# Kernel tuning notes

Measured on AMD Instinct MI355X. Metric: run time of the kernel, lower is better.

## Reference

```python
import jax, jax.numpy as jnp
import numpy as np

K = 5        # kernel_size
S = 1        # stride_size
EPS = 1e-5   # LayerNorm eps (torch default)


def setup_inputs() -> dict:
    key = jax.random.key(0)
    ks = jax.random.split(key, 5)
    N, C, H, W = 8, 512, 32, 32
    O = 512
    x = jax.random.normal(ks[0], (N, C, H, W), dtype=jnp.float32)
    # Linear params (torch.nn.Linear style: y = x @ W.T + b)
    proj_w = jax.random.normal(ks[1], (O, C), dtype=jnp.float32) / np.sqrt(C)
    proj_b = jax.random.normal(ks[2], (O,), dtype=jnp.float32) * 0.01
    score_w = jax.random.normal(ks[3], (1, C), dtype=jnp.float32) / np.sqrt(C)
    score_b = jax.random.normal(ks[4], (1,), dtype=jnp.float32) * 0.01
    # LayerNorm([k*k, 1]) affine params (default init: ones / zeros)
    ln_w = jnp.ones((K * K, 1), dtype=jnp.float32)
    ln_b = jnp.zeros((K * K, 1), dtype=jnp.float32)
    return {"x": x, "proj_w": proj_w, "proj_b": proj_b,
            "score_w": score_w, "score_b": score_b,
            "ln_w": ln_w, "ln_b": ln_b}


def reference(x, proj_w, proj_b, score_w, score_b, ln_w, ln_b):
    N, C, H, W = x.shape
    O = proj_w.shape[0]
    # torch does reshape (NOT permute) from [N,C,H,W] -> [N,H,W,C]
    xr = x.reshape(N, H, W, C)
    proj = xr @ proj_w.T + proj_b          # [N,H,W,O]
    score = xr @ score_w.T + score_b       # [N,H,W,1]

    Hh = (H - K) // S + 1
    Ww = (W - K) // S + 1
    ri = (jnp.arange(Hh) * S)[:, None] + jnp.arange(K)   # [Hh,K]
    ci = (jnp.arange(Ww) * S)[:, None] + jnp.arange(K)   # [Ww,K]
    # im2col-style gather of all windows at once
    p = proj[:, ri[:, None, :, None], ci[None, :, None, :], :]   # [N,Hh,Ww,K,K,O]
    p = p.reshape(N, Hh, Ww, K * K, O)
    sc = score[:, ri[:, None, :, None], ci[None, :, None, :], :] # [N,Hh,Ww,K,K,1]
    sc = sc.reshape(N, Hh, Ww, K * K, 1)

    # LayerNorm over normalized_shape=[K*K, 1] (last two axes)
    mu = jnp.mean(sc, axis=(-2, -1), keepdims=True)
    var = jnp.var(sc, axis=(-2, -1), keepdims=True)
    scn = (sc - mu) * jax.lax.rsqrt(var + EPS) * ln_w + ln_b

    w_attn = jax.nn.softmax(scn, axis=-2)                # softmax over K*K axis
    out = jnp.sum(p * w_attn, axis=-2)                   # [N,Hh,Ww,O]
    # torch stacking order yields [N, O, Hh, Ww]
    return jnp.transpose(out, (0, 3, 1, 2))
```

## Files before the change

kernel.cpp:

```cpp
#include <hip/hip_runtime.h>

typedef __bf16 bf16_t;
typedef bf16_t bf16x8 __attribute__((ext_vector_type(8)));
typedef float  f32x4  __attribute__((ext_vector_type(4)));

#define GAS __attribute__((address_space(1)))
#define LAS __attribute__((address_space(3)))

static constexpr int Nn = 8, Cc = 512, Hi = 32, Wi = 32, Oo = 512;
static constexpr int HO = 28, WO = 28;
static constexpr int NPOS = HO * WO;
static constexpr int MY = Nn * NPOS;
static constexpr int M_ROWS = Nn * Hi * Wi;

__device__ __forceinline__ float bf2f(unsigned short u) {
  union { unsigned int i; float f; } v; v.i = ((unsigned int)u) << 16; return v.f;
}
__device__ __forceinline__ unsigned short f2bf(float f) {
  union { float f; unsigned int u; } v; v.f = f;
  unsigned int u = v.u;
  return (unsigned short)((u + 0x7fffu + ((u >> 16) & 1u)) >> 16);
}
__device__ __forceinline__ uint4 pack8(float4 f0, float4 f1) {
  uint4 r;
  r.x = (unsigned)f2bf(f0.x) | ((unsigned)f2bf(f0.y) << 16);
  r.y = (unsigned)f2bf(f0.z) | ((unsigned)f2bf(f0.w) << 16);
  r.z = (unsigned)f2bf(f1.x) | ((unsigned)f2bf(f1.y) << 16);
  r.w = (unsigned)f2bf(f1.z) | ((unsigned)f2bf(f1.w) << 16);
  return r;
}

__global__ __launch_bounds__(256) void prep_kern(
    const float* __restrict__ X, const float* __restrict__ Wf,
    const float* __restrict__ Sw, const float* __restrict__ Sb,
    unsigned short* __restrict__ Wb, float* __restrict__ S)
{
  const int lane = threadIdx.x & 63;
  const int wave = threadIdx.x >> 6;
  const int bid  = blockIdx.x;
  if (bid < M_ROWS / 4) {
    const int m = bid * 4 + wave;
    const float* xf = X + (size_t)m * Cc + lane * 8;
    const float4 x0 = *(const float4*)xf, x1 = *(const float4*)(xf + 4);
    const float* wf = Sw + lane * 8;
    const float4 w0 = *(const float4*)wf, w1 = *(const float4*)(wf + 4);
    float s = x0.x * w0.x + x0.y * w0.y + x0.z * w0.z + x0.w * w0.w
            + x1.x * w1.x + x1.y * w1.y + x1.z * w1.z + x1.w * w1.w;
    #pragma unroll
    for (int off = 32; off > 0; off >>= 1) s += __shfl_down(s, off, 64);
    if (lane == 0) S[m] = s + Sb[0];
  } else {
    const int r = (bid - M_ROWS / 4) * 4 + wave;
    const float* wf = Wf + (size_t)r * Cc + lane * 8;
    const float4 f0 = *(const float4*)wf, f1 = *(const float4*)(wf + 4);
    *(uint4*)(Wb + (size_t)r * Cc + lane * 8) = pack8(f0, f1);
  }
}

__global__ __launch_bounds__(256) void attnY_kern(
    const float* __restrict__ X, const float* __restrict__ S,
    const float* __restrict__ lnw, const float* __restrict__ lnb,
    unsigned short* __restrict__ Yt)
{
  const int g = blockIdx.x;
  const int n = blockIdx.y;
  const int t = threadIdx.x;

  __shared__ unsigned short Xt[Hi * Wi * 16];
  __shared__ float sl[Hi * Wi];
  __shared__ float lwv[25], lbv[25];

  #pragma unroll
  for (int itr = 0; itr < 8; itr++) {
    const int id = itr * 256 + t;
    const int row = id >> 1, ch8 = (id & 1) * 8;
    const float* xp = X + ((size_t)n * Hi * Wi + row) * Cc + g * 16 + ch8;
    const float4 f0 = *(const float4*)xp, f1 = *(const float4*)(xp + 4);
    *(uint4*)&Xt[row * 16 + ch8] = pack8(f0, f1);
  }
  #pragma unroll
  for (int k = 0; k < 4; k++) sl[k * 256 + t] = S[n * Hi * Wi + k * 256 + t];
  if (t < 25) { lwv[t] = lnw[t]; lbv[t] = lnb[t]; }
  __syncthreads();

  for (int itp = 0; itp < 4; itp++) {
    const int pos = itp * 256 + t;
    if (pos < NPOS) {
      const int i = pos / WO;
      const int j = pos - i * WO;

      float v[25], mu = 0.f;
      #pragma unroll
      for (int q = 0; q < 25; q++) { v[q] = sl[(i + q / 5) * Wi + j + q % 5]; mu += v[q]; }
      mu *= (1.0f / 25.0f);
      float var = 0.f;
      #pragma unroll
      for (int q = 0; q < 25; q++) { const float d = v[q] - mu; var += d * d; }
      var *= (1.0f / 25.0f);
      const float rr = rsqrtf(var + 1e-5f);
      float mx = -1e30f;
      #pragma unroll
      for (int q = 0; q < 25; q++) { v[q] = (v[q] - mu) * rr * lwv[q] + lbv[q]; mx = fmaxf(mx, v[q]); }
      float den = 0.f;
      #pragma unroll
      for (int q = 0; q < 25; q++) { v[q] = __expf(v[q] - mx); den += v[q]; }
      const float inv = 1.0f / den;

      float acc[16];
      #pragma unroll
      for (int c = 0; c < 16; c++) acc[c] = 0.f;
      #pragma unroll
      for (int ki = 0; ki < 5; ki++) {
        const int rb = (i + ki) * Wi + j;
        #pragma unroll
        for (int kj = 0; kj < 5; kj++) {
          const uint4* pr = (const uint4*)&Xt[(rb + kj) * 16];
          const uint4 a = pr[0], b = pr[1];
          const float wv = v[ki * 5 + kj] * inv;
          acc[0]  += bf2f((unsigned short)(a.x & 0xFFFFu)) * wv;
          acc[1]  += bf2f((unsigned short)(a.x >> 16)) * wv;
          acc[2]  += bf2f((unsigned short)(a.y & 0xFFFFu)) * wv;
          acc[3]  += bf2f((unsigned short)(a.y >> 16)) * wv;
          acc[4]  += bf2f((unsigned short)(a.z & 0xFFFFu)) * wv;
          acc[5]  += bf2f((unsigned short)(a.z >> 16)) * wv;
          acc[6]  += bf2f((unsigned short)(a.w & 0xFFFFu)) * wv;
          acc[7]  += bf2f((unsigned short)(a.w >> 16)) * wv;
          acc[8]  += bf2f((unsigned short)(b.x & 0xFFFFu)) * wv;
          acc[9]  += bf2f((unsigned short)(b.x >> 16)) * wv;
          acc[10] += bf2f((unsigned short)(b.y & 0xFFFFu)) * wv;
          acc[11] += bf2f((unsigned short)(b.y >> 16)) * wv;
          acc[12] += bf2f((unsigned short)(b.z & 0xFFFFu)) * wv;
          acc[13] += bf2f((unsigned short)(b.z >> 16)) * wv;
          acc[14] += bf2f((unsigned short)(b.w & 0xFFFFu)) * wv;
          acc[15] += bf2f((unsigned short)(b.w >> 16)) * wv;
        }
      }
      unsigned short* yp = Yt + ((size_t)g * MY + n * NPOS + pos) * 16;
      uint4 o0, o1;
      o0.x = (unsigned)f2bf(acc[0])  | ((unsigned)f2bf(acc[1])  << 16);
      o0.y = (unsigned)f2bf(acc[2])  | ((unsigned)f2bf(acc[3])  << 16);
      o0.z = (unsigned)f2bf(acc[4])  | ((unsigned)f2bf(acc[5])  << 16);
      o0.w = (unsigned)f2bf(acc[6])  | ((unsigned)f2bf(acc[7])  << 16);
      o1.x = (unsigned)f2bf(acc[8])  | ((unsigned)f2bf(acc[9])  << 16);
      o1.y = (unsigned)f2bf(acc[10]) | ((unsigned)f2bf(acc[11]) << 16);
      o1.z = (unsigned)f2bf(acc[12]) | ((unsigned)f2bf(acc[13]) << 16);
      o1.w = (unsigned)f2bf(acc[14]) | ((unsigned)f2bf(acc[15]) << 16);
      *(uint4*)yp = o0;
      *(uint4*)(yp + 8) = o1;
    }
  }
}

#define BM 128
#define BN 64
#define BK 32

__global__ __launch_bounds__(256) void gemm_out(
    const unsigned short* __restrict__ Yt, const bf16_t* __restrict__ Wb,
    const float* __restrict__ Bp, float* __restrict__ out)
{
  __shared__ bf16_t lA[BM * BK];
  __shared__ bf16_t lB[BN * BK];
  const int t    = threadIdx.x;
  const int bm   = blockIdx.x;
  const int bn   = blockIdx.y;
  const int lane = t & 63;
  const int wave = t >> 6;
  const int wm   = (wave >> 1) * 64;
  const int wn   = (wave & 1) * 32;

  f32x4 acc[4][2];
  #pragma unroll
  for (int a = 0; a < 4; a++)
    #pragma unroll
    for (int b = 0; b < 2; b++) acc[a][b] = (f32x4){0.f, 0.f, 0.f, 0.f};

  const int r0 = t >> 2;
  const int c0 = (t & 3) * 8;
  const int rrA = bm * BM + r0;
  const bf16_t* Bg = Wb + (size_t)(bn * BN + r0) * Cc + c0;

  for (int k0 = 0; k0 < Cc; k0 += BK) {
    const int kk = k0 + c0;
    const unsigned short* Ag0 = Yt + ((size_t)(kk >> 4) * MY + rrA) * 16 + (kk & 15);
    __syncthreads();
    __builtin_amdgcn_global_load_lds((const GAS void*)Ag0,              (LAS void*)&lA[t * 8],         16, 0, 0);
    __builtin_amdgcn_global_load_lds((const GAS void*)(Ag0 + 64 * 16),  (LAS void*)&lA[(t + 256) * 8], 16, 0, 0);
    __builtin_amdgcn_global_load_lds((const GAS void*)(Bg + k0),        (LAS void*)&lB[t * 8],         16, 0, 0);
    __syncthreads();

    const int kof = (lane >> 4) * 8;
    bf16x8 af[4], bfr[2];
    #pragma unroll
    for (int mt = 0; mt < 4; mt++)
      af[mt] = *(const bf16x8*)&lA[(wm + mt * 16 + (lane & 15)) * BK + kof];
    #pragma unroll
    for (int nt = 0; nt < 2; nt++)
      bfr[nt] = *(const bf16x8*)&lB[(wn + nt * 16 + (lane & 15)) * BK + kof];
    #pragma unroll
    for (int mt = 0; mt < 4; mt++)
      #pragma unroll
      for (int nt = 0; nt < 2; nt++)
        acc[mt][nt] = __builtin_amdgcn_mfma_f32_16x16x32_bf16(af[mt], bfr[nt], acc[mt][nt], 0, 0, 0);
  }

  #pragma unroll
  for (int nt = 0; nt < 2; nt++) {
    const int col = bn * BN + wn + nt * 16 + (lane & 15);
    const float bias = Bp[col];
    #pragma unroll
    for (int mt = 0; mt < 4; mt++) {
      const int rr0 = bm * BM + wm + mt * 16 + (lane >> 4) * 4;
      const int n0  = rr0 / NPOS;
      const int pos0 = rr0 - n0 * NPOS;
      float4 q;
      q.x = acc[mt][nt][0] + bias;
      q.y = acc[mt][nt][1] + bias;
      q.z = acc[mt][nt][2] + bias;
      q.w = acc[mt][nt][3] + bias;
      *(float4*)&out[((size_t)n0 * Oo + col) * NPOS + pos0] = q;
    }
  }
}

extern "C" void kernel_launch(void* const* d_in, const int* in_sizes, int n_in,
                              void* d_out, int out_size, void* d_ws, size_t ws_size,
                              hipStream_t stream) {
  const float* x   = (const float*)d_in[0];
  const float* pw  = (const float*)d_in[1];
  const float* pb  = (const float*)d_in[2];
  const float* sw  = (const float*)d_in[3];
  const float* sb  = (const float*)d_in[4];
  const float* lnw = (const float*)d_in[5];
  const float* lnb = (const float*)d_in[6];

  char* w = (char*)d_ws;
  float*          Sv = (float*)w;
  unsigned short* Wb = (unsigned short*)(w + (64 << 10));
  unsigned short* Yt = (unsigned short*)(w + (1 << 20));

  prep_kern<<<dim3(M_ROWS / 4 + Oo / 4), 256, 0, stream>>>(x, pw, sw, sb, Wb, Sv);
  attnY_kern<<<dim3(Oo / 16, Nn), 256, 0, stream>>>(x, Sv, lnw, lnb, Yt);
  gemm_out<<<dim3(MY / BM, Oo / BN), 256, 0, stream>>>(Yt, (const bf16_t*)Wb, pb, (float*)d_out);
}
```

Measured before the change: 109.4 us.

## Halve GEMM M-tile and stage output through LDS for coalesced stores

Reduces the output GEMM block tile from 128 to 64 rows, doubling the number of workgroups and halving per-wave accumulators. The epilogue now writes accumulators into a padded LDS tile and then stores each output column with 64 consecutive positions per wave, replacing scattered float4 stores along the NCHW output. This aims to improve occupancy and store coalescing. In exchange, every B tile is loaded twice as often and the epilogue adds an LDS round trip and an extra barrier.

```diff
diff --git a/kernel.cpp b/kernel.cpp
--- a/kernel.cpp
+++ b/kernel.cpp
@@ -151,7 +151,7 @@
   }
 }
 
-#define BM 128
+#define BM 64
 #define BN 64
 #define BK 32
 
@@ -161,17 +161,18 @@
 {
   __shared__ bf16_t lA[BM * BK];
   __shared__ bf16_t lB[BN * BK];
+  __shared__ float  ldsC[BM * 65];
   const int t    = threadIdx.x;
   const int bm   = blockIdx.x;
   const int bn   = blockIdx.y;
   const int lane = t & 63;
   const int wave = t >> 6;
-  const int wm   = (wave >> 1) * 64;
+  const int wm   = (wave >> 1) * 32;
   const int wn   = (wave & 1) * 32;
 
-  f32x4 acc[4][2];
-  #pragma unroll
-  for (int a = 0; a < 4; a++)
+  f32x4 acc[2][2];
+  #pragma unroll
+  for (int a = 0; a < 2; a++)
     #pragma unroll
     for (int b = 0; b < 2; b++) acc[a][b] = (f32x4){0.f, 0.f, 0.f, 0.f};
 
@@ -184,42 +185,46 @@
     const int kk = k0 + c0;
     const unsigned short* Ag0 = Yt + ((size_t)(kk >> 4) * MY + rrA) * 16 + (kk & 15);
     __syncthreads();
-    __builtin_amdgcn_global_load_lds((const GAS void*)Ag0,              (LAS void*)&lA[t * 8],         16, 0, 0);
-    __builtin_amdgcn_global_load_lds((const GAS void*)(Ag0 + 64 * 16),  (LAS void*)&lA[(t + 256) * 8], 16, 0, 0);
-    __builtin_amdgcn_global_load_lds((const GAS void*)(Bg + k0),        (LAS void*)&lB[t * 8],         16, 0, 0);
+    __builtin_amdgcn_global_load_lds((const GAS void*)Ag0, (LAS void*)&lA[t * 8], 16, 0, 0);
+    __builtin_amdgcn_global_load_lds((const GAS void*)Bg,  (LAS void*)&lB[t * 8], 16, 0, 0);
+    Bg += BK;
     __syncthreads();
 
     const int kof = (lane >> 4) * 8;
-    bf16x8 af[4], bfr[2];
-    #pragma unroll
-    for (int mt = 0; mt < 4; mt++)
+    bf16x8 af[2], bfr[2];
+    #pragma unroll
+    for (int mt = 0; mt < 2; mt++)
       af[mt] = *(const bf16x8*)&lA[(wm + mt * 16 + (lane & 15)) * BK + kof];
     #pragma unroll
     for (int nt = 0; nt < 2; nt++)
       bfr[nt] = *(const bf16x8*)&lB[(wn + nt * 16 + (lane & 15)) * BK + kof];
     #pragma unroll
-    for (int mt = 0; mt < 4; mt++)
+    for (int mt = 0; mt < 2; mt++)
       #pragma unroll
       for (int nt = 0; nt < 2; nt++)
         acc[mt][nt] = __builtin_amdgcn_mfma_f32_16x16x32_bf16(af[mt], bfr[nt], acc[mt][nt], 0, 0, 0);
   }
 
   #pragma unroll
-  for (int nt = 0; nt < 2; nt++) {
-    const int col = bn * BN + wn + nt * 16 + (lane & 15);
-    const float bias = Bp[col];
-    #pragma unroll
-    for (int mt = 0; mt < 4; mt++) {
-      const int rr0 = bm * BM + wm + mt * 16 + (lane >> 4) * 4;
-      const int n0  = rr0 / NPOS;
-      const int pos0 = rr0 - n0 * NPOS;
-      float4 q;
-      q.x = acc[mt][nt][0] + bias;
-      q.y = acc[mt][nt][1] + bias;
-      q.z = acc[mt][nt][2] + bias;
-      q.w = acc[mt][nt][3] + bias;
-      *(float4*)&out[((size_t)n0 * Oo + col) * NPOS + pos0] = q;
+  for (int mt = 0; mt < 2; mt++)
+    #pragma unroll
+    for (int nt = 0; nt < 2; nt++) {
+      const int row = wm + mt * 16 + (lane >> 4) * 4;
+      const int col = wn + nt * 16 + (lane & 15);
+      #pragma unroll
+      for (int r = 0; r < 4; r++)
+        ldsC[(row + r) * 65 + col] = acc[mt][nt][r];
     }
+  __syncthreads();
+
+  const int rr  = bm * BM + lane;
+  const int n0  = rr / NPOS;
+  const int pos0 = rr - n0 * NPOS;
+  #pragma unroll
+  for (int cc = 0; cc < 16; cc++) {
+    const int col = bn * BN + wave * 16 + cc;
+    const float val = ldsC[lane * 65 + wave * 16 + cc] + Bp[col];
+    out[(size_t)(n0 * Oo + col) * NPOS + pos0] = val;
   }
 }
 
```

After: 108.5 us. About the same (-0.8%).
